# Performance work log

Hardware: AMD Instinct MI355X
Metric: run time of the kernel (lower is better)

The kernel has to match this reference:

```python
import jax, jax.numpy as jnp
import numpy as np

N_EXPERTS, D_IN, D_OUT = 8, 1024, 1024
N_TOKENS = 8192


def setup_inputs() -> dict:
    key = jax.random.key(0)
    ks = jax.random.split(key, 5)
    s_in = 1.0 / np.sqrt(D_IN)
    x = jax.random.normal(ks[0], (N_TOKENS, D_IN), dtype=jnp.float32)
    W = jax.random.uniform(ks[1], (N_EXPERTS, D_IN, D_OUT), jnp.float32, -s_in, s_in)
    b = jax.random.uniform(ks[2], (N_EXPERTS, D_OUT), jnp.float32, -s_in, s_in)
    gate_W = jax.random.uniform(ks[3], (D_IN, N_EXPERTS), jnp.float32, -s_in, s_in)
    gate_b = jax.random.uniform(ks[4], (N_EXPERTS,), jnp.float32, -s_in, s_in)
    return {"x": x, "W": W, "b": b, "gate_W": gate_W, "gate_b": gate_b}


def reference(x, W, b, gate_W, gate_b):
    # gate: [n, e] softmax over experts
    gate_score = jax.nn.softmax(x @ gate_W + gate_b, axis=-1)
    # all experts applied densely: [n, e, o]
    expert_outputs = jnp.einsum('ni,eio->neo', x, W) + b[None, :, :]
    # weighted combine over expert axis: [n, o]
    return jnp.einsum('ne,neo->no', gate_score, expert_outputs)
```

## Files before the change

kernel.cpp:

```cpp
#include <hip/hip_runtime.h>
#include <hip/hip_bf16.h>
#include <cstdint>
#include <cstddef>

#define N_TOK 8192
#define D_IN  1024
#define D_OUT 1024
#define N_EXP 8
#define KTOT  (N_EXP * D_IN)

typedef __attribute__((ext_vector_type(8))) short short8;
typedef __attribute__((ext_vector_type(8))) unsigned short ushort8;
typedef __attribute__((ext_vector_type(4))) float f32x4;

__device__ __forceinline__ unsigned short f2bf(float f) {
    union { float f; unsigned int u; } v; v.f = f;
    return (unsigned short)((v.u + 0x7FFFu + ((v.u >> 16) & 1u)) >> 16);
}

__device__ __forceinline__ void load_lds16(const void* g, void* l) {
    __builtin_amdgcn_global_load_lds(
        (const __attribute__((address_space(1))) void*)g,
        (__attribute__((address_space(3))) void*)l,
        16, 0, 0);
}

__global__ __launch_bounds__(256) void prep_kernel(
    const float* __restrict__ x, const float* __restrict__ gW,
    const float* __restrict__ gbias, const float* __restrict__ W,
    unsigned short* __restrict__ xb, unsigned short* __restrict__ Wt,
    float* __restrict__ g_t) {
    const int b = blockIdx.x;
    const int t = threadIdx.x;

    if (b < 2048) {
        __shared__ float tile[64][65];
        const int e  = b >> 8;
        const int i0 = ((b >> 4) & 15) * 64;
        const int o0 = (b & 15) * 64;

        const int rr = t >> 4;
        const int rc = (t & 15) * 4;
#pragma unroll
        for (int j = 0; j < 4; ++j) {
            const float4 v = *(const float4*)(
                W + ((size_t)e * D_IN + (i0 + rr + 16 * j)) * D_OUT + o0 + rc);
            tile[rr + 16 * j][rc + 0] = v.x;
            tile[rr + 16 * j][rc + 1] = v.y;
            tile[rr + 16 * j][rc + 2] = v.z;
            tile[rr + 16 * j][rc + 3] = v.w;
        }
        __syncthreads();
        const int ow = t >> 2;
        const int c  = (t & 3) * 16;
        ushort8 v0, v1;
#pragma unroll
        for (int j = 0; j < 8; ++j) v0[j] = f2bf(tile[c + j][ow]);
#pragma unroll
        for (int j = 0; j < 8; ++j) v1[j] = f2bf(tile[c + 8 + j][ow]);
        unsigned short* dst = Wt + (size_t)(o0 + ow) * KTOT + e * D_IN + i0 + c;
        *(ushort8*)dst = v0;
        *(ushort8*)(dst + 8) = v1;
    } else {
        const int lane = t & 63;
        const int n    = (b - 2048) * 4 + (t >> 6);

        float acc[8];
#pragma unroll
        for (int e = 0; e < 8; ++e) acc[e] = 0.f;
#pragma unroll
        for (int jj = 0; jj < 4; ++jj) {
            const int i = 256 * jj + 4 * lane;
            const float4 xv = *(const float4*)(x + (size_t)n * D_IN + i);
            ushort4 u;
            u.x = f2bf(xv.x); u.y = f2bf(xv.y);
            u.z = f2bf(xv.z); u.w = f2bf(xv.w);
            *(ushort4*)(xb + (size_t)n * D_IN + i) = u;
            const float xs[4] = {xv.x, xv.y, xv.z, xv.w};
#pragma unroll
            for (int j = 0; j < 4; ++j) {
                const float* wr = gW + (size_t)(i + j) * N_EXP;
                const float4 w0 = *(const float4*)wr;
                const float4 w1 = *(const float4*)(wr + 4);
                acc[0] += xs[j] * w0.x; acc[1] += xs[j] * w0.y;
                acc[2] += xs[j] * w0.z; acc[3] += xs[j] * w0.w;
                acc[4] += xs[j] * w1.x; acc[5] += xs[j] * w1.y;
                acc[6] += xs[j] * w1.z; acc[7] += xs[j] * w1.w;
            }
        }
#pragma unroll
        for (int off = 32; off > 0; off >>= 1) {
#pragma unroll
            for (int e = 0; e < 8; ++e) acc[e] += __shfl_down(acc[e], off);
        }
        if (lane == 0) {
            float lg[8], mx = -1e30f;
#pragma unroll
            for (int e = 0; e < 8; ++e) {
                lg[e] = acc[e] + gbias[e];
                mx = fmaxf(mx, lg[e]);
            }
            float s = 0.f;
#pragma unroll
            for (int e = 0; e < 8; ++e) { lg[e] = expf(lg[e] - mx); s += lg[e]; }
            const float inv = 1.f / s;
#pragma unroll
            for (int e = 0; e < 8; ++e)
                g_t[(size_t)e * N_TOK + n] = lg[e] * inv;
        }
    }
}

__global__ __launch_bounds__(256, 2) void moe_gemm6_kernel(
    const unsigned short* __restrict__ xb,
    const unsigned short* __restrict__ Wt,
    const float* __restrict__ bias,
    const float* __restrict__ g_t,
    float* __restrict__ out) {
    __shared__ __align__(16) unsigned short Abuf[2][128 * 32];
    __shared__ __align__(16) unsigned short Bbuf[2][128 * 32];
    __shared__ __align__(16) float g_s[N_EXP][128];
    __shared__ __align__(16) float r_s[N_EXP][128];
    __shared__ __align__(16) float b_s[N_EXP][128];

    const int t    = threadIdx.x;
    const int lane = t & 63;
    const int ln15 = lane & 15;
    const int quad = lane >> 4;
    const int wave = t >> 6;
    const int wm0  = (wave >> 1) * 64;
    const int wn0  = (wave & 1) * 64;

    const int flat = blockIdx.x + 8 * blockIdx.y;
    const int xs_  = (flat >> 3) & 7;
    const int ys_  = ((flat & 7) << 3) | (flat >> 6);
    const int bn0  = xs_ * 128;
    const int bm0  = ys_ * 128;

    for (int j = t; j < N_EXP * 128; j += 256) {
        const int e = j >> 7, r = j & 127;
        g_s[e][r] = g_t[(size_t)e * N_TOK + bm0 + r];
        b_s[e][r] = bias[(size_t)e * D_OUT + bn0 + r];
    }
    __syncthreads();
    if (t < 128) {
        float d[N_EXP];
#pragma unroll
        for (int e = 0; e < N_EXP; ++e) d[e] = fmaxf(g_s[e][t], 1e-30f);
#pragma unroll
        for (int e = 1; e < N_EXP; ++e) r_s[e][t] = d[e - 1] / d[e];
        r_s[0][t] = d[N_EXP - 1];
    }

    f32x4 acc[4][4];
#pragma unroll
    for (int mi = 0; mi < 4; ++mi)
#pragma unroll
        for (int ni = 0; ni < 4; ++ni)
            acc[mi][ni] = (f32x4){0.f, 0.f, 0.f, 0.f};

    unsigned short* aL0[2] = {&Abuf[0][wave * 512], &Abuf[1][wave * 512]};
    unsigned short* aL1[2] = {&Abuf[0][2048 + wave * 512],
                              &Abuf[1][2048 + wave * 512]};
    unsigned short* bL0[2] = {&Bbuf[0][wave * 512], &Bbuf[1][wave * 512]};
    unsigned short* bL1[2] = {&Bbuf[0][2048 + wave * 512],
                              &Bbuf[1][2048 + wave * 512]};

    const int csw = ((t & 3) ^ ((t >> 3) & 3)) * 8;
    const unsigned short* ga =
        xb + (size_t)(bm0 + (t >> 2)) * D_IN + csw;
    const unsigned short* gbB =
        Wt + (size_t)(bn0 + (t >> 2)) * KTOT + csw;

    const int ksw = (quad ^ ((ln15 >> 1) & 3)) * 8;

    load_lds16(ga, aL0[0]);
    load_lds16(ga + 64 * D_IN, aL1[0]);
    load_lds16(gbB, bL0[0]);
    load_lds16(gbB + 64 * KTOT, bL1[0]);
    __syncthreads();

    for (int kt = 0; kt < 256; ++kt) {
        const int cb  = kt & 1;
        const int nb  = cb ^ 1;
        const int kt1 = (kt + 1) & 255;

        load_lds16(ga + (kt1 & 31) * 32,              aL0[nb]);
        load_lds16(ga + 64 * D_IN + (kt1 & 31) * 32,  aL1[nb]);
        load_lds16(gbB + kt1 * 32,                    bL0[nb]);
        load_lds16(gbB + 64 * KTOT + kt1 * 32,        bL1[nb]);

        if (kt && !(kt & 31)) {
            const int e = kt >> 5;
#pragma unroll
            for (int mi = 0; mi < 4; ++mi) {
                const f32x4 rv = *(const f32x4*)&r_s[e][wm0 + mi * 16 + quad * 4];
#pragma unroll
                for (int ni = 0; ni < 4; ++ni)
#pragma unroll
                    for (int r = 0; r < 4; ++r) acc[mi][ni][r] *= rv[r];
            }
        }

        short8 af[4], bv[4];
#pragma unroll
        for (int mi = 0; mi < 4; ++mi)
            af[mi] = *(const short8*)
                &Abuf[cb][(wm0 + mi * 16 + ln15) * 32 + ksw];
#pragma unroll
        for (int ni = 0; ni < 4; ++ni)
            bv[ni] = *(const short8*)
                &Bbuf[cb][(wn0 + ni * 16 + ln15) * 32 + ksw];
#pragma unroll
        for (int mi = 0; mi < 4; ++mi)
#pragma unroll
            for (int ni = 0; ni < 4; ++ni)
                acc[mi][ni] = __builtin_amdgcn_mfma_f32_16x16x32_bf16(
                    af[mi], bv[ni], acc[mi][ni], 0, 0, 0);

        __syncthreads();
    }

#pragma unroll
    for (int mi = 0; mi < 4; ++mi) {
        const f32x4 fin = *(const f32x4*)&r_s[0][wm0 + mi * 16 + quad * 4];
#pragma unroll
        for (int ni = 0; ni < 4; ++ni)
#pragma unroll
            for (int r = 0; r < 4; ++r) acc[mi][ni][r] *= fin[r];
    }
#pragma unroll
    for (int e = 0; e < N_EXP; ++e) {
        f32x4 gv[4];
        float bv[4];
#pragma unroll
        for (int mi = 0; mi < 4; ++mi)
            gv[mi] = *(const f32x4*)&g_s[e][wm0 + mi * 16 + quad * 4];
#pragma unroll
        for (int ni = 0; ni < 4; ++ni) bv[ni] = b_s[e][wn0 + ni * 16 + ln15];
#pragma unroll
        for (int mi = 0; mi < 4; ++mi)
#pragma unroll
            for (int ni = 0; ni < 4; ++ni)
#pragma unroll
                for (int r = 0; r < 4; ++r)
                    acc[mi][ni][r] += gv[mi][r] * bv[ni];
    }

#pragma unroll
    for (int mi = 0; mi < 4; ++mi) {
#pragma unroll
        for (int ni = 0; ni < 4; ++ni) {
            const int col  = bn0 + wn0 + ni * 16 + ln15;
            const int row0 = bm0 + wm0 + mi * 16 + quad * 4;
#pragma unroll
            for (int r = 0; r < 4; ++r)
                out[(size_t)(row0 + r) * D_OUT + col] = acc[mi][ni][r];
        }
    }
}

extern "C" void kernel_launch(void* const* d_in, const int* in_sizes, int n_in,
                              void* d_out, int out_size, void* d_ws, size_t ws_size,
                              hipStream_t stream) {
    const float* x  = (const float*)d_in[0];
    const float* W  = (const float*)d_in[1];
    const float* b  = (const float*)d_in[2];
    const float* gW = (const float*)d_in[3];
    const float* gb = (const float*)d_in[4];
    float* out = (float*)d_out;

    unsigned short* xb  = (unsigned short*)d_ws;
    unsigned short* Wt  = xb + (size_t)N_TOK * D_IN;
    float*          g_t = (float*)(Wt + (size_t)D_OUT * KTOT);

    prep_kernel<<<4096, 256, 0, stream>>>(x, gW, gb, W, xb, Wt, g_t);
    moe_gemm6_kernel<<<dim3(D_OUT / 128, N_TOK / 128), 256, 0, stream>>>(
        xb, Wt, b, g_t, out);
}
```

Before: 287.2 us.

## Enlarge GEMM tile to 256x128 with 512 threads and 4-stage LDS pipeline

The MoE GEMM kernel now uses a 256x128 block tile with 8 waves and a 4-slot LDS ring buffer that prefetches three k-steps ahead. Waits use explicit vmcnt counts, and MFMA issue is wrapped in s_setprio. The goal is to hide global-load latency better and to reuse each B tile across more rows. The grouped block swizzle is removed and the grid shrinks to 256 blocks. Larger LDS use and 512 threads may limit occupancy, and 256 blocks may leave compute units underused.

```diff
diff --git a/kernel.cpp b/kernel.cpp
--- a/kernel.cpp
+++ b/kernel.cpp
@@ -8,6 +8,11 @@
 #define D_OUT 1024
 #define N_EXP 8
 #define KTOT  (N_EXP * D_IN)
+
+#define BM    256
+#define BN    128
+#define BKH   32
+#define NSTEP 256
 
 typedef __attribute__((ext_vector_type(8))) short short8;
 typedef __attribute__((ext_vector_type(8))) unsigned short ushort8;
@@ -111,17 +116,17 @@
     }
 }
 
-__global__ __launch_bounds__(256, 2) void moe_gemm6_kernel(
+__global__ __launch_bounds__(512, 2) void moe_gemm8_kernel(
     const unsigned short* __restrict__ xb,
     const unsigned short* __restrict__ Wt,
     const float* __restrict__ bias,
     const float* __restrict__ g_t,
     float* __restrict__ out) {
-    __shared__ __align__(16) unsigned short Abuf[2][128 * 32];
-    __shared__ __align__(16) unsigned short Bbuf[2][128 * 32];
-    __shared__ __align__(16) float g_s[N_EXP][128];
-    __shared__ __align__(16) float r_s[N_EXP][128];
-    __shared__ __align__(16) float b_s[N_EXP][128];
+    __shared__ __align__(16) unsigned short A4[4][BM * BKH];
+    __shared__ __align__(16) unsigned short B4[4][BN * BKH];
+    __shared__ __align__(16) float g_s[N_EXP][BM];
+    __shared__ __align__(16) float r_s[N_EXP][BM];
+    __shared__ __align__(16) float b_s[N_EXP][BN];
 
     const int t    = threadIdx.x;
     const int lane = t & 63;
@@ -131,19 +136,15 @@
     const int wm0  = (wave >> 1) * 64;
     const int wn0  = (wave & 1) * 64;
 
-    const int flat = blockIdx.x + 8 * blockIdx.y;
-    const int xs_  = (flat >> 3) & 7;
-    const int ys_  = ((flat & 7) << 3) | (flat >> 6);
-    const int bn0  = xs_ * 128;
-    const int bm0  = ys_ * 128;
-
-    for (int j = t; j < N_EXP * 128; j += 256) {
-        const int e = j >> 7, r = j & 127;
-        g_s[e][r] = g_t[(size_t)e * N_TOK + bm0 + r];
-        b_s[e][r] = bias[(size_t)e * D_OUT + bn0 + r];
-    }
+    const int bn0 = blockIdx.x * BN;
+    const int bm0 = blockIdx.y * BM;
+
+    for (int j = t; j < N_EXP * BM; j += 512)
+        g_s[j >> 8][j & 255] = g_t[(size_t)(j >> 8) * N_TOK + bm0 + (j & 255)];
+    for (int j = t; j < N_EXP * BN; j += 512)
+        b_s[j >> 7][j & 127] = bias[(size_t)(j >> 7) * D_OUT + bn0 + (j & 127)];
     __syncthreads();
-    if (t < 128) {
+    if (t < BM) {
         float d[N_EXP];
 #pragma unroll
         for (int e = 0; e < N_EXP; ++e) d[e] = fmaxf(g_s[e][t], 1e-30f);
@@ -151,6 +152,7 @@
         for (int e = 1; e < N_EXP; ++e) r_s[e][t] = d[e - 1] / d[e];
         r_s[0][t] = d[N_EXP - 1];
     }
+    __syncthreads();
 
     f32x4 acc[4][4];
 #pragma unroll
@@ -159,67 +161,80 @@
         for (int ni = 0; ni < 4; ++ni)
             acc[mi][ni] = (f32x4){0.f, 0.f, 0.f, 0.f};
 
-    unsigned short* aL0[2] = {&Abuf[0][wave * 512], &Abuf[1][wave * 512]};
-    unsigned short* aL1[2] = {&Abuf[0][2048 + wave * 512],
-                              &Abuf[1][2048 + wave * 512]};
-    unsigned short* bL0[2] = {&Bbuf[0][wave * 512], &Bbuf[1][wave * 512]};
-    unsigned short* bL1[2] = {&Bbuf[0][2048 + wave * 512],
-                              &Bbuf[1][2048 + wave * 512]};
-
-    const int csw = ((t & 3) ^ ((t >> 3) & 3)) * 8;
-    const unsigned short* ga =
-        xb + (size_t)(bm0 + (t >> 2)) * D_IN + csw;
-    const unsigned short* gbB =
-        Wt + (size_t)(bn0 + (t >> 2)) * KTOT + csw;
-
-    const int ksw = (quad ^ ((ln15 >> 1) & 3)) * 8;
-
-    load_lds16(ga, aL0[0]);
-    load_lds16(ga + 64 * D_IN, aL1[0]);
-    load_lds16(gbB, bL0[0]);
-    load_lds16(gbB + 64 * KTOT, bL1[0]);
-    __syncthreads();
-
-    for (int kt = 0; kt < 256; ++kt) {
-        const int cb  = kt & 1;
-        const int nb  = cb ^ 1;
-        const int kt1 = (kt + 1) & 255;
-
-        load_lds16(ga + (kt1 & 31) * 32,              aL0[nb]);
-        load_lds16(ga + 64 * D_IN + (kt1 & 31) * 32,  aL1[nb]);
-        load_lds16(gbB + kt1 * 32,                    bL0[nb]);
-        load_lds16(gbB + 64 * KTOT + kt1 * 32,        bL1[nb]);
-
-        if (kt && !(kt & 31)) {
-            const int e = kt >> 5;
-#pragma unroll
-            for (int mi = 0; mi < 4; ++mi) {
-                const f32x4 rv = *(const f32x4*)&r_s[e][wm0 + mi * 16 + quad * 4];
-#pragma unroll
-                for (int ni = 0; ni < 4; ++ni)
-#pragma unroll
-                    for (int r = 0; r < 4; ++r) acc[mi][ni][r] *= rv[r];
-            }
-        }
-
-        short8 af[4], bv[4];
-#pragma unroll
-        for (int mi = 0; mi < 4; ++mi)
-            af[mi] = *(const short8*)
-                &Abuf[cb][(wm0 + mi * 16 + ln15) * 32 + ksw];
-#pragma unroll
-        for (int ni = 0; ni < 4; ++ni)
-            bv[ni] = *(const short8*)
-                &Bbuf[cb][(wn0 + ni * 16 + ln15) * 32 + ksw];
-#pragma unroll
-        for (int mi = 0; mi < 4; ++mi)
-#pragma unroll
-            for (int ni = 0; ni < 4; ++ni)
-                acc[mi][ni] = __builtin_amdgcn_mfma_f32_16x16x32_bf16(
-                    af[mi], bv[ni], acc[mi][ni], 0, 0, 0);
-
-        __syncthreads();
-    }
+    const int srow = t >> 2;
+    const int csw  = ((t & 3) ^ ((t >> 3) & 3)) * 8;
+    const unsigned short* gA = xb + (size_t)(bm0 + srow) * D_IN + csw;
+    const unsigned short* gB = Wt + (size_t)(bn0 + srow) * (size_t)KTOT + csw;
+    const int wrow = wave * 16 * BKH;
+
+    const int ksw  = (quad ^ ((ln15 >> 1) & 3)) * 8;
+    const int aoff = (wm0 + ln15) * BKH + ksw;
+    const int boff = (wn0 + ln15) * BKH + ksw;
+
+#pragma unroll
+    for (int s = 0; s < 3; ++s) {
+        load_lds16(gA + s * BKH,              &A4[s][wrow]);
+        load_lds16(gA + 128 * D_IN + s * BKH, &A4[s][128 * BKH + wrow]);
+        load_lds16(gB + (size_t)s * BKH,      &B4[s][wrow]);
+    }
+    asm volatile("s_waitcnt vmcnt(6)" ::: "memory");
+    __builtin_amdgcn_s_barrier();
+    __builtin_amdgcn_sched_barrier(0);
+
+#define HALF_STEP(h_, DO_STAGE)                                               \
+  {                                                                           \
+    const int slot_ = (h_) & 3;                                               \
+    const unsigned short* Ab_ = &A4[slot_][0];                                \
+    const unsigned short* Bb_ = &B4[slot_][0];                                \
+    const int hs_ = (h_) + 3;                                                 \
+    if ((h_) && !((h_) & 31)) {      \
+      const int e_ = (h_) >> 5;                                               \
+      _Pragma("unroll") for (int mi = 0; mi < 4; ++mi) {                      \
+        const f32x4 rv = *(const f32x4*)&r_s[e_][wm0 + mi * 16 + quad * 4];   \
+        _Pragma("unroll") for (int ni = 0; ni < 4; ++ni)                      \
+          _Pragma("unroll") for (int r = 0; r < 4; ++r)                       \
+            acc[mi][ni][r] *= rv[r];                                          \
+      }                                                                       \
+    }                                                                         \
+    short8 af_[4], bv_[4];                                                    \
+    _Pragma("unroll") for (int mi = 0; mi < 4; ++mi)                          \
+      af_[mi] = *(const short8*)(Ab_ + aoff + mi * 16 * BKH);                 \
+    _Pragma("unroll") for (int ni = 0; ni < 4; ++ni)                          \
+      bv_[ni] = *(const short8*)(Bb_ + boff + ni * 16 * BKH);                 \
+    if (DO_STAGE) {                                                           \
+      load_lds16(gA + ((hs_) & 31) * BKH,              &A4[(hs_) & 3][wrow]); \
+      load_lds16(gA + 128 * D_IN + ((hs_) & 31) * BKH,                        \
+                 &A4[(hs_) & 3][128 * BKH + wrow]);                           \
+      load_lds16(gB + (size_t)(hs_) * BKH,             &B4[(hs_) & 3][wrow]); \
+    }                                                                         \
+    __builtin_amdgcn_s_barrier();                                             \
+    asm volatile("s_waitcnt lgkmcnt(0)" ::: "memory");                        \
+    __builtin_amdgcn_sched_barrier(0);                                        \
+    __builtin_amdgcn_s_setprio(1);                                            \
+    _Pragma("unroll") for (int mi = 0; mi < 4; ++mi)                          \
+      _Pragma("unroll") for (int ni = 0; ni < 4; ++ni)                        \
+        acc[mi][ni] = __builtin_amdgcn_mfma_f32_16x16x32_bf16(                \
+            af_[mi], bv_[ni], acc[mi][ni], 0, 0, 0);                          \
+    __builtin_amdgcn_s_setprio(0);                                            \
+  }
+
+#define END_WAIT(N_)                                                          \
+  asm volatile("s_waitcnt vmcnt(" #N_ ")" ::: "memory");                      \
+  __builtin_amdgcn_s_barrier();                                               \
+  __builtin_amdgcn_sched_barrier(0);
+
+    for (int h = 0; h < NSTEP - 3; ++h) {
+        HALF_STEP(h, 1);
+        END_WAIT(6);
+    }
+    HALF_STEP(253, 0);
+    END_WAIT(3);
+    HALF_STEP(254, 0);
+    END_WAIT(0);
+    HALF_STEP(255, 0);
+
+#undef HALF_STEP
+#undef END_WAIT
 
 #pragma unroll
     for (int mi = 0; mi < 4; ++mi) {
@@ -232,19 +247,19 @@
 #pragma unroll
     for (int e = 0; e < N_EXP; ++e) {
         f32x4 gv[4];
-        float bv[4];
+        float bb[4];
 #pragma unroll
         for (int mi = 0; mi < 4; ++mi)
             gv[mi] = *(const f32x4*)&g_s[e][wm0 + mi * 16 + quad * 4];
 #pragma unroll
-        for (int ni = 0; ni < 4; ++ni) bv[ni] = b_s[e][wn0 + ni * 16 + ln15];
+        for (int ni = 0; ni < 4; ++ni) bb[ni] = b_s[e][wn0 + ni * 16 + ln15];
 #pragma unroll
         for (int mi = 0; mi < 4; ++mi)
 #pragma unroll
             for (int ni = 0; ni < 4; ++ni)
 #pragma unroll
                 for (int r = 0; r < 4; ++r)
-                    acc[mi][ni][r] += gv[mi][r] * bv[ni];
+                    acc[mi][ni][r] += gv[mi][r] * bb[ni];
     }
 
 #pragma unroll
@@ -275,6 +290,6 @@
     float*          g_t = (float*)(Wt + (size_t)D_OUT * KTOT);
 
     prep_kernel<<<4096, 256, 0, stream>>>(x, gW, gb, W, xb, Wt, g_t);
-    moe_gemm6_kernel<<<dim3(D_OUT / 128, N_TOK / 128), 256, 0, stream>>>(
+    moe_gemm8_kernel<<<dim3(D_OUT / BN, N_TOK / BM), 512, 0, stream>>>(
         xb, Wt, b, g_t, out);
 }
```

Measured after the change: 295.4 us. 2.9% more time.
